# Kernel optimization log

Hardware: AMD Instinct MI355X
Metric: run time of the kernel (lower is better)

Reference implementation:

```python
import jax, jax.numpy as jnp
import numpy as np

N, C = 4194304, 8
EPS = 1.0
T_LAMBDA = 1.0
T_CM = EPS * -0.5
T_STD = 0.75
F_CM = 0.8
F_STD = 0.85
T_MU = jnp.array([[0.5], [0.5]], dtype=jnp.float32)   # [2,1]
F_MU = jnp.array([[0.3], [0.15]], dtype=jnp.float32)  # [2,1]
T_COV = jnp.array([[T_STD, T_CM], [T_CM, T_STD]], dtype=jnp.float32)
F_COV = jnp.array([[F_STD, F_CM], [F_CM, F_STD]], dtype=jnp.float32)


def setup_inputs() -> dict:
    key = jax.random.key(0)
    k1, k2 = jax.random.split(key)
    inputs = jax.random.normal(k1, (N, C), dtype=jnp.float32)
    targets = jax.random.randint(k2, (N,), 0, C, dtype=jnp.int64)
    return {"inputs": inputs, "targets": targets}


def _co_gau(sv, cov, mu):
    # sv: [2, N]. Original computes diag(diff.T @ inv_cov @ diff); we compute the
    # diagonal directly (same values, O(N) memory instead of O(N^2)).
    diff = sv - mu                                      # [2, N]
    inv_cov = jnp.linalg.inv(cov)                       # [2, 2]
    q = jnp.einsum('in,ij,jn->n', diff, inv_cov, diff)  # [N]
    return jnp.exp(-0.5 * q)


def reference(inputs, targets):
    logp = jax.nn.log_softmax(inputs, axis=1)           # [N, C]
    probs = jnp.exp(logp)
    tgt = targets[:, None]
    ce_loss = -jnp.take_along_axis(logp, tgt, axis=1)[:, 0]   # [N]
    p_t = jnp.take_along_axis(probs, tgt, axis=1)[:, 0]       # [N]
    top2, _ = jax.lax.top_k(probs, 2)                   # [N, 2]
    max_probs = top2[:, 0]
    second_max_probs = top2[:, 1]
    is_pt_max = max_probs == p_t
    p_negative = jnp.where(is_pt_max, second_max_probs, max_probs)
    sv_flat = jnp.stack([p_t, p_negative], axis=0)      # [2, N]
    t_value = T_LAMBDA * _co_gau(sv_flat, T_COV, T_MU)
    f_value = _co_gau(sv_flat, F_COV, F_MU)
    value = jnp.where(is_pt_max, t_value, f_value)
    return (ce_loss * value).mean()
```

## Files before the change

kernel.cpp:

```cpp
#include <hip/hip_runtime.h>


#define N_ROWS 4194304
#define TPB 256
#define GRID 2048
#define RPT (N_ROWS / (GRID * TPB))

__device__ __forceinline__ float row_contrib(float4 v0, float4 v1, int t) {
    const float aT = 2.4f,                bT = 1.6f;
    const float aF = 10.30303030303030f,  bF = -9.69696969696970f;

    float m1 = v0.x, m2 = -INFINITY;
    float xs[7] = {v0.y, v0.z, v0.w, v1.x, v1.y, v1.z, v1.w};
    #pragma unroll
    for (int i = 0; i < 7; ++i) {
        float xi = xs[i];
        float hi = fmaxf(xi, m1);
        float lo = fminf(xi, m1);
        m2 = fmaxf(m2, lo);
        m1 = hi;
    }

    float s = __expf(v0.x - m1) + __expf(v0.y - m1) +
              __expf(v0.z - m1) + __expf(v0.w - m1) +
              __expf(v1.x - m1) + __expf(v1.y - m1) +
              __expf(v1.z - m1) + __expf(v1.w - m1);

    float xt = v0.x;
    xt = (t == 1) ? v0.y : xt;
    xt = (t == 2) ? v0.z : xt;
    xt = (t == 3) ? v0.w : xt;
    xt = (t == 4) ? v1.x : xt;
    xt = (t == 5) ? v1.y : xt;
    xt = (t == 6) ? v1.z : xt;
    xt = (t == 7) ? v1.w : xt;

    float inv_s = 1.0f / s;
    float logs  = __logf(s);
    float p_t   = __expf(xt - m1) * inv_s;
    float ce    = (m1 - xt) + logs;

    bool  is_t  = (xt == m1);
    float p2    = __expf(m2 - m1) * inv_s;
    float pmax  = inv_s;
    float p_neg = is_t ? p2 : pmax;

    float a  = is_t ? aT : aF;
    float b  = is_t ? bT : bF;
    float dx = p_t   - (is_t ? 0.5f : 0.3f);
    float dy = p_neg - (is_t ? 0.5f : 0.15f);

    float q = a * (dx * dx + dy * dy) + 2.0f * b * dx * dy;
    return ce * __expf(-0.5f * q);
}

__global__ __launch_bounds__(TPB) void coga_stage1(
    const float4* __restrict__ x4,
    const int* __restrict__ tgt,
    float* __restrict__ partials)
{
    const int tid    = blockIdx.x * TPB + threadIdx.x;
    const int stride = GRID * TPB;

    float acc = 0.0f;
    #pragma unroll
    for (int k = 0; k < RPT; k += 4) {
        float4 a0[4], a1[4];
        int    t[4];
        #pragma unroll
        for (int j = 0; j < 4; ++j) {
            size_t row = (size_t)tid + (size_t)(k + j) * stride;
            a0[j] = x4[2 * row];
            a1[j] = x4[2 * row + 1];
            t[j]  = tgt[row];
        }
        #pragma unroll
        for (int j = 0; j < 4; ++j)
            acc += row_contrib(a0[j], a1[j], t[j]);
    }

    #pragma unroll
    for (int off = 32; off > 0; off >>= 1)
        acc += __shfl_down(acc, off, 64);

    __shared__ float wsum[TPB / 64];
    int lane = threadIdx.x & 63;
    int wid  = threadIdx.x >> 6;
    if (lane == 0) wsum[wid] = acc;
    __syncthreads();

    if (threadIdx.x == 0) {
        float bs = 0.0f;
        #pragma unroll
        for (int w = 0; w < TPB / 64; ++w) bs += wsum[w];
        partials[blockIdx.x] = bs;
    }
}

__global__ __launch_bounds__(1024) void coga_stage2(
    const float* __restrict__ partials,
    float* __restrict__ out)
{
    float s = 0.0f;
    for (int i = threadIdx.x; i < GRID; i += 1024)
        s += partials[i];

    #pragma unroll
    for (int off = 32; off > 0; off >>= 1)
        s += __shfl_down(s, off, 64);

    __shared__ float wsum[1024 / 64];
    int lane = threadIdx.x & 63;
    int wid  = threadIdx.x >> 6;
    if (lane == 0) wsum[wid] = s;
    __syncthreads();

    if (threadIdx.x == 0) {
        float bs = 0.0f;
        #pragma unroll
        for (int w = 0; w < 1024 / 64; ++w) bs += wsum[w];
        out[0] = bs * (1.0f / (float)N_ROWS);
    }
}

__global__ __launch_bounds__(TPB) void coga_fallback(
    const float* __restrict__ x,
    const int* __restrict__ tgt,
    float* __restrict__ out)
{
    float acc = 0.0f;
    int stride = gridDim.x * TPB;
    for (int row = blockIdx.x * TPB + threadIdx.x; row < N_ROWS; row += stride) {
        const float4* p = (const float4*)(x + (size_t)row * 8);
        acc += row_contrib(p[0], p[1], tgt[row]);
    }
    #pragma unroll
    for (int off = 32; off > 0; off >>= 1)
        acc += __shfl_down(acc, off, 64);
    __shared__ float wsum[TPB / 64];
    int lane = threadIdx.x & 63;
    int wid  = threadIdx.x >> 6;
    if (lane == 0) wsum[wid] = acc;
    __syncthreads();
    if (threadIdx.x == 0) {
        float bs = 0.0f;
        #pragma unroll
        for (int w = 0; w < TPB / 64; ++w) bs += wsum[w];
        atomicAdd(out, bs * (1.0f / (float)N_ROWS));
    }
}

extern "C" void kernel_launch(void* const* d_in, const int* in_sizes, int n_in,
                              void* d_out, int out_size, void* d_ws, size_t ws_size,
                              hipStream_t stream) {
    const float* x   = (const float*)d_in[0];
    const int*   tgt = (const int*)d_in[1];
    float*       out = (float*)d_out;

    if (ws_size >= GRID * sizeof(float)) {
        float* partials = (float*)d_ws;
        coga_stage1<<<GRID, TPB, 0, stream>>>((const float4*)x, tgt, partials);
        coga_stage2<<<1, 1024, 0, stream>>>(partials, out);
    } else {
        hipMemsetAsync(out, 0, sizeof(float), stream);
        coga_fallback<<<512, TPB, 0, stream>>>(x, tgt, out);
    }
}
```

Measured before the change: 199.9 us.

## Split each row across lane pairs for fully coalesced float4 loads

Each row of 8 floats is now handled by two adjacent lanes, each loading one contiguous float4, so a wave reads a contiguous span instead of a 32-byte stride per lane. Row max, second max, exp-sum and the target logit are combined through xor-shuffles. Targets are loaded once per wave and broadcast with shuffles. Both lanes compute the same row contribution, so the final scale is halved. In exchange the transcendental and tail math is computed twice per row and extra shuffle instructions are added.

```diff
diff --git a/kernel.cpp b/kernel.cpp
--- a/kernel.cpp
+++ b/kernel.cpp
@@ -4,36 +4,28 @@
 #define N_ROWS 4194304
 #define TPB 256
 #define GRID 2048
-#define RPT (N_ROWS / (GRID * TPB))
+#define ROWS_PER_BLOCK (N_ROWS / GRID)
+#define ITERS (ROWS_PER_BLOCK / TPB)
 
-__device__ __forceinline__ float row_contrib(float4 v0, float4 v1, int t) {
-    const float aT = 2.4f,                bT = 1.6f;
-    const float aF = 10.30303030303030f,  bF = -9.69696969696970f;
-
-    float m1 = v0.x, m2 = -INFINITY;
-    float xs[7] = {v0.y, v0.z, v0.w, v1.x, v1.y, v1.z, v1.w};
-    #pragma unroll
-    for (int i = 0; i < 7; ++i) {
-        float xi = xs[i];
-        float hi = fmaxf(xi, m1);
-        float lo = fminf(xi, m1);
-        m2 = fmaxf(m2, lo);
-        m1 = hi;
-    }
-
-    float s = __expf(v0.x - m1) + __expf(v0.y - m1) +
-              __expf(v0.z - m1) + __expf(v0.w - m1) +
-              __expf(v1.x - m1) + __expf(v1.y - m1) +
-              __expf(v1.z - m1) + __expf(v1.w - m1);
-
-    float xt = v0.x;
-    xt = (t == 1) ? v0.y : xt;
-    xt = (t == 2) ? v0.z : xt;
-    xt = (t == 3) ? v0.w : xt;
-    xt = (t == 4) ? v1.x : xt;
-    xt = (t == 5) ? v1.y : xt;
-    xt = (t == 6) ? v1.z : xt;
-    xt = (t == 7) ? v1.w : xt;
+__device__ __forceinline__ float pair_contrib(float4 h, int t, int half) {
+    float a = fmaxf(h.x, h.y), b = fminf(h.x, h.y);
+    float c = fmaxf(h.z, h.w), d = fminf(h.z, h.w);
+    float m1L = fmaxf(a, c);
+    float m2L = fmaxf(fminf(a, c), fmaxf(b, d));
+    float m1P = __shfl_xor(m1L, 1, 64);
+    float m2P = __shfl_xor(m2L, 1, 64);
+    float m1 = fmaxf(m1L, m1P);
+    float m2 = fmaxf(fminf(m1L, m1P), fmaxf(m2L, m2P));
+    float sL = __expf(h.x - m1) + __expf(h.y - m1) +
+               __expf(h.z - m1) + __expf(h.w - m1);
+    float s = sL + __shfl_xor(sL, 1, 64);
+    int tc = t & 3;
+    float cand = h.x;
+    cand = (tc == 1) ? h.y : cand;
+    cand = (tc == 2) ? h.z : cand;
+    cand = (tc == 3) ? h.w : cand;
+    float xm = ((t >> 2) == half) ? cand : 0.0f;
+    float xt = xm + __shfl_xor(xm, 1, 64);
 
     float inv_s = 1.0f / s;
     float logs  = __logf(s);
@@ -42,15 +34,14 @@
 
     bool  is_t  = (xt == m1);
     float p2    = __expf(m2 - m1) * inv_s;
-    float pmax  = inv_s;
-    float p_neg = is_t ? p2 : pmax;
+    float p_neg = is_t ? p2 : inv_s;
 
-    float a  = is_t ? aT : aF;
-    float b  = is_t ? bT : bF;
+    float aC = is_t ? 2.4f : 10.30303030303030f;
+    float bC = is_t ? 1.6f : -9.69696969696970f;
     float dx = p_t   - (is_t ? 0.5f : 0.3f);
     float dy = p_neg - (is_t ? 0.5f : 0.15f);
 
-    float q = a * (dx * dx + dy * dy) + 2.0f * b * dx * dy;
+    float q = aC * (dx * dx + dy * dy) + 2.0f * bC * dx * dy;
     return ce * __expf(-0.5f * q);
 }
 
@@ -59,24 +50,24 @@
     const int* __restrict__ tgt,
     float* __restrict__ partials)
 {
-    const int tid    = blockIdx.x * TPB + threadIdx.x;
-    const int stride = GRID * TPB;
+    const int wave = threadIdx.x >> 6;
+    const int lane = threadIdx.x & 63;
+    const int half = lane & 1;
+
+    const size_t block_row0 = (size_t)blockIdx.x * ROWS_PER_BLOCK;
 
     float acc = 0.0f;
     #pragma unroll
-    for (int k = 0; k < RPT; k += 4) {
-        float4 a0[4], a1[4];
-        int    t[4];
-        #pragma unroll
-        for (int j = 0; j < 4; ++j) {
-            size_t row = (size_t)tid + (size_t)(k + j) * stride;
-            a0[j] = x4[2 * row];
-            a1[j] = x4[2 * row + 1];
-            t[j]  = tgt[row];
-        }
-        #pragma unroll
-        for (int j = 0; j < 4; ++j)
-            acc += row_contrib(a0[j], a1[j], t[j]);
+    for (int i = 0; i < ITERS; ++i) {
+        size_t row0 = block_row0 + (size_t)i * TPB + (size_t)wave * 64;
+        size_t b4 = row0 * 2;
+        float4 h0 = x4[b4 + lane];
+        float4 h1 = x4[b4 + 64 + lane];
+        int t_all = tgt[row0 + lane];
+        int t0 = __shfl(t_all, lane >> 1, 64);
+        int t1 = __shfl(t_all, 32 + (lane >> 1), 64);
+        acc += pair_contrib(h0, t0, half);
+        acc += pair_contrib(h1, t1, half);
     }
 
     #pragma unroll
@@ -84,9 +75,7 @@
         acc += __shfl_down(acc, off, 64);
 
     __shared__ float wsum[TPB / 64];
-    int lane = threadIdx.x & 63;
-    int wid  = threadIdx.x >> 6;
-    if (lane == 0) wsum[wid] = acc;
+    if (lane == 0) wsum[wave] = acc;
     __syncthreads();
 
     if (threadIdx.x == 0) {
@@ -119,8 +108,44 @@
         float bs = 0.0f;
         #pragma unroll
         for (int w = 0; w < 1024 / 64; ++w) bs += wsum[w];
-        out[0] = bs * (1.0f / (float)N_ROWS);
+        out[0] = bs * (0.5f / (float)N_ROWS);
     }
+}
+
+__device__ __forceinline__ float row_contrib(float4 v0, float4 v1, int t) {
+    float m1 = v0.x, m2 = -INFINITY;
+    float xs[7] = {v0.y, v0.z, v0.w, v1.x, v1.y, v1.z, v1.w};
+    #pragma unroll
+    for (int i = 0; i < 7; ++i) {
+        float xi = xs[i];
+        float hi = fmaxf(xi, m1);
+        float lo = fminf(xi, m1);
+        m2 = fmaxf(m2, lo);
+        m1 = hi;
+    }
+    float s = __expf(v0.x - m1) + __expf(v0.y - m1) +
+              __expf(v0.z - m1) + __expf(v0.w - m1) +
+              __expf(v1.x - m1) + __expf(v1.y - m1) +
+              __expf(v1.z - m1) + __expf(v1.w - m1);
+    float xt = v0.x;
+    xt = (t == 1) ? v0.y : xt;
+    xt = (t == 2) ? v0.z : xt;
+    xt = (t == 3) ? v0.w : xt;
+    xt = (t == 4) ? v1.x : xt;
+    xt = (t == 5) ? v1.y : xt;
+    xt = (t == 6) ? v1.z : xt;
+    xt = (t == 7) ? v1.w : xt;
+    float inv_s = 1.0f / s;
+    float p_t   = __expf(xt - m1) * inv_s;
+    float ce    = (m1 - xt) + __logf(s);
+    bool  is_t  = (xt == m1);
+    float p_neg = is_t ? __expf(m2 - m1) * inv_s : inv_s;
+    float aC = is_t ? 2.4f : 10.30303030303030f;
+    float bC = is_t ? 1.6f : -9.69696969696970f;
+    float dx = p_t   - (is_t ? 0.5f : 0.3f);
+    float dy = p_neg - (is_t ? 0.5f : 0.15f);
+    float q = aC * (dx * dx + dy * dy) + 2.0f * bC * dx * dy;
+    return ce * __expf(-0.5f * q);
 }
 
 __global__ __launch_bounds__(TPB) void coga_fallback(
```

Result: slower. 203.9 us (+2.0%).
